# Kernel tuning notes

Hardware: AMD Instinct MI355X
Metric: run time of the kernel (lower is better)

The kernel has to match this reference:

```python
import jax, jax.numpy as jnp
import numpy as np
import functools

N, D, R, E, L, C, MAXDEG = 40000, 128, 3, 640000, 2, 40, 512
BN_EPS = 1e-5


def setup_inputs():
    ks = iter(jax.random.split(jax.random.key(0), 40))
    nrm = lambda s, sc=0.05: jax.random.normal(next(ks), s, dtype=jnp.float32) * sc
    x = jax.random.normal(next(ks), (N, D), dtype=jnp.float32)
    edge_indices = jax.random.randint(next(ks), (R, 2, E), 0, N, dtype=jnp.int32)
    out_emb = nrm((L, MAXDEG, D)).at[:, 0].set(0.0)  # padding_idx=0 -> zero row
    in_emb = nrm((L, MAXDEG, D)).at[:, 0].set(0.0)
    return dict(
        x=x, edge_indices=edge_indices,
        W_src=nrm((L, D, D)), b_src=nrm((L, D)),
        W_dst=nrm((L, D, D)), b_dst=nrm((L, D)),
        W_outf=nrm((L, D)), b_outf=nrm((L,)),
        W_inf=nrm((L, D)), b_inf=nrm((L,)),
        W_fc=nrm((L, D, D)), b_fc=nrm((L, D)),
        bn_gamma=jnp.ones((L, D), jnp.float32), bn_beta=jnp.zeros((L, D), jnp.float32),
        out_deg_emb=out_emb, in_deg_emb=in_emb,
        out_mask=jnp.ones((R, N), jnp.float32), out_mask_bias=jnp.zeros((R, N), jnp.float32),
        in_mask=jnp.ones((R, N), jnp.float32), in_mask_bias=jnp.zeros((R, N), jnp.float32),
        alpha=jnp.float32(0.5), tau=jnp.float32(0.0),
        W_lin=nrm((D, C)), b_lin=nrm((C,)),
    )


def _forward(x, W_src, b_src, W_dst, b_dst, W_outf, b_outf, W_inf, b_inf,
             W_fc, b_fc, bn_gamma, bn_beta, out_deg_emb, in_deg_emb,
             out_mask, out_mask_bias, in_mask, in_mask_bias, alpha, tau,
             W_lin, b_lin, edge_indices):
    seg = lambda d, i: jax.ops.segment_sum(d, i, num_segments=N)
    # source builds I with arange(0, N-1): identity with last diagonal entry missing
    i_mask = (jnp.arange(N) < N - 1).astype(jnp.float32)[:, None]

    rel = []
    for r in range(R):
        row, col = edge_indices[r, 0], edge_indices[r, 1]
        ones = jnp.ones(E, jnp.float32)
        out_deg, in_deg = seg(ones, row), seg(ones, col)
        ods = jnp.where(out_deg > 0, 1.0 / jnp.sqrt(jnp.maximum(out_deg, 1.0)), 0.0)
        ids_ = jnp.where(in_deg > 0, 1.0 / jnp.sqrt(jnp.maximum(in_deg, 1.0)), 0.0)
        # 'dir' norm: D_out^{-1/2} A D_in^{-1/2}; the transposed adj shares the same edge weights
        w = ods[row] * ids_[col]
        rel.append((row, col, w,
                    jnp.clip(out_deg, 0, MAXDEG - 1).astype(jnp.int32),
                    jnp.clip(in_deg, 0, MAXDEG - 1).astype(jnp.int32)))

    def spmm(r_, y):  # adj_norm @ y : gather cols, scatter-add to rows
        row, col, w = rel[r_][0], rel[r_][1], rel[r_][2]
        return seg(w[:, None] * y[col], row)

    def spmm_t(r_, y):  # adj_norm^T @ y
        row, col, w = rel[r_][0], rel[r_][1], rel[r_][2]
        return seg(w[:, None] * y[row], col)

    def dirichlet(mm, y):
        x1 = y / (jnp.sum(jnp.abs(y), axis=1, keepdims=True) + 1e-12)  # row_l1_normalize
        x1sq = x1 * x1
        return (i_mask * x1sq + mm(x1sq)) - 2.0 * ((i_mask * x1 + mm(x1)) * x1 - x1sq)

    eff_tau = jnp.exp(tau) + 0.1

    def conv(l, h):
        out = jnp.zeros((N, D), h.dtype)
        cis, cos_ = [], []
        for r in range(R):
            mm = functools.partial(spmm, r)
            mmt = functools.partial(spmm_t, r)
            out_nei, in_nei = mm(h), mmt(h)
            e_out, e_in = dirichlet(mm, h), dirichlet(mmt, h)
            c_out = (-e_out + out_deg_emb[l][rel[r][3]]) @ W_outf[l] + b_outf[l]  # [N]
            c_in = (-e_in + in_deg_emb[l][rel[r][4]]) @ W_inf[l] + b_inf[l]
            cm = jax.nn.softmax(jnp.stack([c_out, c_in], axis=1) / eff_tau, axis=1)  # tau_softmax
            c_out = cm[:, 0] * out_mask[r] + out_mask_bias[r]
            c_in = cm[:, 1] * in_mask[r] + in_mask_bias[r]
            out = out + c_out[:, None] * (out_nei @ W_src[l] + b_src[l]) \
                      + c_in[:, None] * (in_nei @ W_dst[l] + b_dst[l])
            cis.append(c_in)
            cos_.append(c_out)
        out = out / R
        # F.pad(x,(0,dim-x.shape[1])) is a no-op since input_dim == output_dim
        output = out + alpha * (h @ W_fc[l] + b_fc[l])
        mu, var = jnp.mean(output, axis=0), jnp.var(output, axis=0)  # BatchNorm1d (train mode)
        output = (output - mu) / jnp.sqrt(var + BN_EPS) * bn_gamma[l] + bn_beta[l]
        return output, jnp.mean(jnp.stack(cis), 0)[:, None], jnp.mean(jnp.stack(cos_), 0)[:, None]

    pos_h, neg_h = x, x
    pos_hs, neg_hs, gs, cins, couts = [], [], [], [], []
    for l in range(L):
        ph, ci, co = conv(l, pos_h)
        ph = jax.nn.relu(ph)  # jumping_knowledge truthy -> relu every layer; dropout p=0
        perm = jax.random.permutation(jax.random.key(100 + l), N)  # torch.randperm
        nh, _, _ = conv(l, neg_h[perm])
        nh = jax.nn.relu(nh)
        pos_h, neg_h = ph, nh
        pos_hs.append(ph)
        neg_hs.append(nh)
        gs.append(jnp.mean(ph, axis=0, keepdims=True))
        cins.append(ci)
        couts.append(co)
    c_ins = jnp.mean(jnp.stack(cins), 0)
    c_outs = jnp.mean(jnp.stack(couts), 0)
    jk = functools.reduce(jnp.maximum, pos_hs)  # JumpingKnowledge mode='max'
    logp = jax.nn.log_softmax(jk @ W_lin + b_lin, axis=1)
    return (logp, c_ins, c_outs, *pos_hs, *neg_hs, *gs)


def reference(x, edge_indices, W_src, b_src, W_dst, b_dst, W_outf, b_outf,
              W_inf, b_inf, W_fc, b_fc, bn_gamma, bn_beta, out_deg_emb,
              in_deg_emb, out_mask, out_mask_bias, in_mask, in_mask_bias,
              alpha, tau, W_lin, b_lin):
    return _forward(x, W_src, b_src, W_dst, b_dst, W_outf, b_outf, W_inf, b_inf,
                    W_fc, b_fc, bn_gamma, bn_beta, out_deg_emb, in_deg_emb,
                    out_mask, out_mask_bias, in_mask, in_mask_bias, alpha, tau,
                    W_lin, b_lin, edge_indices)
```

## Files before the change

kernel.cpp:

```cpp
#include <hip/hip_runtime.h>

constexpr int Nn = 40000;
constexpr int Dd = 128;
constexpr int Rr = 3;
constexpr int Ee = 640000;
constexpr int Ll = 2;
constexpr int Cc = 40;
constexpr int MAXD = 512;
constexpr float BN_EPS = 1e-5f;

constexpr int RB_ELEMS = 1024;
constexpr int RB_NB = (Nn + RB_ELEMS - 1) / RB_ELEMS;
constexpr int RB_BINS = 256;
constexpr int RB_H = RB_BINS * RB_NB;

constexpr int EB_ELEMS = 4096;
constexpr int EB_NB = (Ee + EB_ELEMS - 1) / EB_ELEMS;
constexpr int EB_H = 256 * EB_NB;

constexpr int HR_BINS = 13334;
constexpr int HR_PAD = 13344;
constexpr int HR_SB = 16;
constexpr int HR_CHUNK = (Ee + HR_SB - 1) / HR_SB;

__device__ __forceinline__ unsigned rotl32(unsigned x, int d) { return (x << d) | (x >> (32 - d)); }

__device__ void threefry2x32(unsigned k0, unsigned k1, unsigned c0, unsigned c1,
                             unsigned& o0, unsigned& o1) {
  unsigned ks2 = k0 ^ k1 ^ 0x1BD11BDAu;
  unsigned x0 = c0 + k0, x1 = c1 + k1;
#define TFR4(a,b,c,d2) \
  x0 += x1; x1 = rotl32(x1,a);  x1 ^= x0; \
  x0 += x1; x1 = rotl32(x1,b);  x1 ^= x0; \
  x0 += x1; x1 = rotl32(x1,c);  x1 ^= x0; \
  x0 += x1; x1 = rotl32(x1,d2); x1 ^= x0;
  TFR4(13,15,26,6);  x0 += k1;  x1 += ks2 + 1u;
  TFR4(17,29,16,24); x0 += ks2; x1 += k0 + 2u;
  TFR4(13,15,26,6);  x0 += k0;  x1 += k1 + 3u;
  TFR4(17,29,16,24); x0 += k1;  x1 += ks2 + 4u;
  TFR4(13,15,26,6);  x0 += ks2; x1 += k0 + 5u;
#undef TFR4
  o0 = x0; o1 = x1;
}

__global__ void k_genkeys2(unsigned* __restrict__ keys, unsigned seed0, unsigned seed1,
                           int rounds, int* __restrict__ vout, int doIota) {
  int i = blockIdx.x * blockDim.x + threadIdx.x;
  if (i >= 2 * Nn) return;
  int seg = i / Nn, li = i - seg * Nn;
  unsigned seed = seg ? seed1 : seed0;
  unsigned k0 = 0u, k1 = seed, sk0 = 0u, sk1 = 0u;
  for (int rd = 0; rd < rounds; rd++) {
    unsigned a0, a1, b0, b1;
    threefry2x32(k0, k1, 0u, 0u, a0, a1);
    threefry2x32(k0, k1, 0u, 1u, b0, b1);
    sk0 = b0; sk1 = b1;
    k0 = a0; k1 = a1;
  }
  unsigned o0, o1;
  threefry2x32(sk0, sk1, 0u, (unsigned)li, o0, o1);
  keys[i] = o0 ^ o1;
  if (doIota) vout[i] = li;
}

__global__ void k_rhist2(const unsigned* __restrict__ keys, int* __restrict__ hist, int shift) {
  __shared__ int lh[RB_BINS];
  int a = blockIdx.x / RB_NB, blk = blockIdx.x % RB_NB;
  const unsigned* src = keys + (size_t)a * Nn;
  int t = threadIdx.x;
  lh[t] = 0;
  __syncthreads();
  int base = blk * RB_ELEMS;
  for (int i = t; i < RB_ELEMS; i += 256) {
    int g = base + i;
    if (g < Nn) atomicAdd(&lh[(src[g] >> shift) & 255], 1);
  }
  __syncthreads();
  hist[(size_t)a * RB_H + t * RB_NB + blk] = lh[t];
}

__device__ void scan_body(const int* cnt, int* off, int n, int items) {
  int t = threadIdx.x;
  int lo = t * items, hi = min(lo + items, n);
  int s = 0;
  for (int i = lo; i < hi; i++) s += cnt[i];
  int lane = t & 63, wid = t >> 6;
  int sc = s;
#pragma unroll
  for (int o = 1; o < 64; o <<= 1) {
    int v = __shfl_up(sc, o);
    if (lane >= o) sc += v;
  }
  __shared__ int wsum[16], woff[16];
  if (lane == 63) wsum[wid] = sc;
  __syncthreads();
  if (t == 0) {
    int a = 0;
    for (int w = 0; w < 16; w++) { woff[w] = a; a += wsum[w]; }
    off[n] = a;
  }
  __syncthreads();
  int run = woff[wid] + sc - s;
  for (int i = lo; i < hi; i++) {
    int v = cnt[i];
    off[i] = run;
    run += v;
  }
}

__global__ __launch_bounds__(1024) void k_scanP(const int* __restrict__ hist, int* __restrict__ esc) {
  int a = blockIdx.x;
  scan_body(hist + (size_t)a * RB_H, esc + (size_t)a * (RB_H + 1), RB_H, (RB_H + 1023) / 1024);
}

__global__ __launch_bounds__(1024) void k_scan6(const int* __restrict__ odeg, const int* __restrict__ ideg,
                                                int* __restrict__ csr_off, int* __restrict__ csc_off) {
  int b = blockIdx.x;
  const int* cnt = (b < 3) ? (odeg + b * Nn) : (ideg + (b - 3) * Nn);
  int* off = (b < 3) ? (csr_off + b * (Nn + 1)) : (csc_off + (b - 3) * (Nn + 1));
  scan_body(cnt, off, Nn, (Nn + 1023) / 1024);
}

__global__ void k_rscatter2(const unsigned* __restrict__ keys, const int* __restrict__ vals,
                            const int* __restrict__ scanned, int shift,
                            unsigned* __restrict__ okeys, int* __restrict__ ovals) {
  __shared__ int running[RB_BINS];
  __shared__ int wcount[4][RB_BINS];
  __shared__ int dbase[RB_BINS];
  int a = blockIdx.x / RB_NB, blk = blockIdx.x % RB_NB;
  const unsigned* ksrc = keys + (size_t)a * Nn;
  const int* vsrc = vals + (size_t)a * Nn;
  unsigned* kdst = okeys + (size_t)a * Nn;
  int* vdst = ovals + (size_t)a * Nn;
  int t = threadIdx.x;
  int lane = t & 63, w = t >> 6;
  running[t] = 0;
  dbase[t] = scanned[(size_t)a * (RB_H + 1) + t * RB_NB + blk];
  int base = blk * RB_ELEMS;
  for (int rnd = 0; rnd < 4; rnd++) {
#pragma unroll
    for (int q = 0; q < 4; q++) wcount[q][t] = 0;
    __syncthreads();
    int g = base + rnd * 256 + t;
    bool valid = g < Nn;
    unsigned key = valid ? ksrc[g] : 0u;
    int d = (key >> shift) & 255;
    unsigned long long bb = __ballot(valid);
    unsigned long long mask = bb;
#pragma unroll
    for (int k = 0; k < 8; k++) {
      bool b = (d >> k) & 1;
      unsigned long long tt = __ballot(b && valid);
      mask &= b ? tt : ~tt;
    }
    mask &= bb;
    int riw = __popcll(mask & ((1ull << lane) - 1ull));
    int cnt_ = __popcll(mask);
    if (valid && riw == 0) wcount[w][d] = cnt_;
    __syncthreads();
    if (valid) {
      int prior = 0;
#pragma unroll
      for (int ww = 0; ww < 4; ww++) if (ww < w) prior += wcount[ww][d];
      int gp = dbase[d] + running[d] + prior + riw;
      kdst[gp] = key;
      vdst[gp] = vsrc[g];
    }
    __syncthreads();
    running[t] += wcount[0][t] + wcount[1][t] + wcount[2][t] + wcount[3][t];
    __syncthreads();
  }
}

__global__ void k_permrows(const float* __restrict__ src, const int* __restrict__ perm,
                           float* __restrict__ dst) {
  int row = blockIdx.x * 8 + (threadIdx.x >> 5);
  int lane = threadIdx.x & 31;
  if (row >= Nn) return;
  int p = perm[row];
  ((float4*)(dst + (size_t)row * Dd))[lane] = ((const float4*)(src + (size_t)p * Dd))[lane];
}

__global__ __launch_bounds__(256) void k_hist2(const int* __restrict__ ei, int* __restrict__ partials) {
  __shared__ int lh[HR_BINS];
  int bid = blockIdx.x;
  int sb = bid % HR_SB;
  int range = (bid / HR_SB) % 3;
  int j = bid / (3 * HR_SB);
  int rel = j >> 1, which = j & 1;
  const int* src = ei + (size_t)rel * 2 * Ee + (size_t)which * Ee;
  int lo = range * HR_BINS;
  for (int i = threadIdx.x; i < HR_BINS; i += 256) lh[i] = 0;
  __syncthreads();
  int e0 = sb * HR_CHUNK, e1 = min(e0 + HR_CHUNK, Ee);
  for (int e = e0 + threadIdx.x; e < e1; e += 256) {
    int v = src[e] - lo;
    if (v >= 0 && v < HR_BINS) atomicAdd(&lh[v], 1);
  }
  __syncthreads();
  int* dst = partials + (size_t)bid * HR_PAD;
  for (int i = threadIdx.x; i < HR_BINS; i += 256) dst[i] = lh[i];
}

__global__ void k_hreduce(const int* __restrict__ partials, int* __restrict__ odeg,
                          int* __restrict__ ideg) {
  int idx = blockIdx.x * 256 + threadIdx.x;
  if (idx >= 6 * Nn) return;
  int j = idx / Nn, bin = idx - j * Nn;
  int range = bin / HR_BINS, off = bin - range * HR_BINS;
  const int* p = partials + (size_t)((j * 3 + range) * HR_SB) * HR_PAD + off;
  int sum = 0;
#pragma unroll
  for (int b = 0; b < HR_SB; b++) sum += p[(size_t)b * HR_PAD];
  int rel = j >> 1;
  (j & 1 ? ideg : odeg)[rel * Nn + bin] = sum;
}

__global__ void k_degnorm(const int* __restrict__ odeg, const int* __restrict__ ideg,
                          float* __restrict__ ods, float* __restrict__ ids,
                          int* __restrict__ odix, int* __restrict__ idix) {
  int idx = blockIdx.x * blockDim.x + threadIdx.x;
  if (idx >= Rr * Nn) return;
  int od = odeg[idx], id_ = ideg[idx];
  ods[idx] = od > 0 ? 1.0f / sqrtf((float)od) : 0.0f;
  ids[idx] = id_ > 0 ? 1.0f / sqrtf((float)id_) : 0.0f;
  odix[idx] = od < MAXD - 1 ? od : MAXD - 1;
  idix[idx] = id_ < MAXD - 1 ? id_ : MAXD - 1;
}

__global__ void k_pack(const int* __restrict__ ei, unsigned* __restrict__ pcsr,
                       unsigned* __restrict__ pcsc) {
  int idx = blockIdx.x * 256 + threadIdx.x;
  if (idx >= 3 * Ee) return;
  int r = idx / Ee, e = idx - r * Ee;
  const int* base = ei + (size_t)r * 2 * Ee;
  unsigned rw = (unsigned)base[e], cl = (unsigned)base[Ee + e];
  pcsr[idx] = (rw << 16) | cl;
  pcsc[idx] = (cl << 16) | rw;
}

__global__ __launch_bounds__(256) void k_ehist(const unsigned* __restrict__ pin,
                                               int* __restrict__ hist, int shift) {
  __shared__ int lh[256];
  int a = blockIdx.x / EB_NB, blk = blockIdx.x % EB_NB;
  const unsigned* src = pin + (size_t)a * Ee;
  lh[threadIdx.x] = 0;
  __syncthreads();
  int base = blk * EB_ELEMS;
  for (int i = threadIdx.x; i < EB_ELEMS; i += 256) {
    int g = base + i;
    if (g < Ee) atomicAdd(&lh[(src[g] >> shift) & 255], 1);
  }
  __syncthreads();
  hist[(size_t)a * EB_H + threadIdx.x * EB_NB + blk] = lh[threadIdx.x];
}

__global__ __launch_bounds__(1024) void k_escan6(const int* __restrict__ hist, int* __restrict__ esc) {
  int a = blockIdx.x;
  scan_body(hist + (size_t)a * EB_H, esc + (size_t)a * (EB_H + 1), EB_H, (EB_H + 1023) / 1024);
}

__global__ __launch_bounds__(256) void k_escatter(const unsigned* __restrict__ pin,
                                                  const int* __restrict__ esc, int shift,
                                                  unsigned* __restrict__ pout) {
  __shared__ int running[256];
  __shared__ int wcount[4][256];
  __shared__ int dbase[256];
  int a = blockIdx.x / EB_NB, blk = blockIdx.x % EB_NB;
  const unsigned* src = pin + (size_t)a * Ee;
  unsigned* dst = pout + (size_t)a * Ee;
  int t = threadIdx.x;
  int lane = t & 63, w = t >> 6;
  running[t] = 0;
  dbase[t] = esc[(size_t)a * (EB_H + 1) + t * EB_NB + blk];
  int base = blk * EB_ELEMS;
  for (int rnd = 0; rnd < 16; rnd++) {
#pragma unroll
    for (int q = 0; q < 4; q++) wcount[q][t] = 0;
    __syncthreads();
    int g = base + rnd * 256 + t;
    bool valid = g < Ee;
    unsigned key = valid ? src[g] : 0u;
    int d = (key >> shift) & 255;
    unsigned long long bb = __ballot(valid);
    unsigned long long mask = bb;
#pragma unroll
    for (int k = 0; k < 8; k++) {
      bool b = (d >> k) & 1;
      unsigned long long tt = __ballot(b && valid);
      mask &= b ? tt : ~tt;
    }
    mask &= bb;
    int riw = __popcll(mask & ((1ull << lane) - 1ull));
    int cnt_ = __popcll(mask);
    if (valid && riw == 0) wcount[w][d] = cnt_;
    __syncthreads();
    if (valid) {
      int prior = 0;
#pragma unroll
      for (int ww = 0; ww < 4; ww++) if (ww < w) prior += wcount[ww][d];
      int gp = dbase[d] + running[d] + prior + riw;
      dst[gp] = key;
    }
    __syncthreads();
    running[t] += wcount[0][t] + wcount[1][t] + wcount[2][t] + wcount[3][t];
    __syncthreads();
  }
}

__global__ void k_rowscalar(const float* __restrict__ h, const float* __restrict__ Wfo,
                            const float* __restrict__ Wfi, float4* __restrict__ aux) {
  int wid = (blockIdx.x * blockDim.x + threadIdx.x) >> 6;
  int lane = threadIdx.x & 63;
  if (wid >= Nn) return;
  float2 a = ((const float2*)(h + (size_t)wid * Dd))[lane];
  float2 wo = ((const float2*)Wfo)[lane];
  float2 wi = ((const float2*)Wfi)[lane];
  float l1 = fabsf(a.x) + fabsf(a.y);
  float so = a.x * a.x * wo.x + a.y * a.y * wo.y;
  float si = a.x * a.x * wi.x + a.y * a.y * wi.y;
#pragma unroll
  for (int o = 32; o; o >>= 1) {
    l1 += __shfl_xor(l1, o);
    so += __shfl_xor(so, o);
    si += __shfl_xor(si, o);
  }
  if (lane == 0) {
    float ri = 1.0f / (l1 + 1e-12f);
    aux[wid] = make_float4(ri, ri * ri * so, ri * ri * si, 0.f);
  }
}

__global__ void k_lut(const float* __restrict__ eo, const float* __restrict__ ei_,
                      const float* __restrict__ Wfo, const float* __restrict__ Wfi,
                      float* __restrict__ luto, float* __restrict__ luti) {
  int wid = (blockIdx.x * blockDim.x + threadIdx.x) >> 6;
  int lane = threadIdx.x & 63;
  if (wid >= MAXD) return;
  float2 a = ((const float2*)(eo + (size_t)wid * Dd))[lane];
  float2 b = ((const float2*)(ei_ + (size_t)wid * Dd))[lane];
  float2 wo = ((const float2*)Wfo)[lane];
  float2 wi = ((const float2*)Wfi)[lane];
  float so = a.x * wo.x + a.y * wo.y;
  float si = b.x * wi.x + b.y * wi.y;
#pragma unroll
  for (int o = 32; o; o >>= 1) { so += __shfl_xor(so, o); si += __shfl_xor(si, o); }
  if (lane == 0) { luto[wid] = so; luti[wid] = si; }
}

__global__ __launch_bounds__(256) void k_csrdir3(
    const int* __restrict__ csr_off, const unsigned* __restrict__ pcsr,
    const int* __restrict__ csc_off, const unsigned* __restrict__ pcsc,
    const float* __restrict__ ods_r, const float* __restrict__ ids_r,
    const float4* __restrict__ aux, const float* __restrict__ h,
    const float* __restrict__ Wfo, const float* __restrict__ Wfi,
    const float* __restrict__ luto, const float* __restrict__ luti,
    const int* __restrict__ odix, const int* __restrict__ idix,
    const float* __restrict__ bo, const float* __restrict__ bi,
    const float* __restrict__ taup,
    const float* __restrict__ omask, const float* __restrict__ omaskb,
    const float* __restrict__ imask, const float* __restrict__ imaskb,
    float* __restrict__ Tout, float* __restrict__ Tin,
    float* __restrict__ sco, float* __restrict__ sci,
    float* __restrict__ co_acc, float* __restrict__ ci_acc,
    int first, int is_pos) {
  __shared__ float lq[4], lp[4], lc[4];
  int t = threadIdx.x;
  int wv = t >> 6, lane = t & 63;
  int dir = wv >> 1;
  int n = blockIdx.x * 2 + (wv & 1);
  const int* off = dir ? csc_off : csr_off;
  const unsigned* nbrp = dir ? pcsc : pcsr;
  const float* scn = dir ? ods_r : ids_r;
  float a_self = (dir ? ids_r : ods_r)[n];
  const float* Wf = dir ? Wfi : Wfo;
  int s0 = off[n], s1 = off[n + 1];
  int hl = lane & 31, half = lane >> 5;
  float4 wf4 = ((const float4*)Wf)[hl];
  float4 hn4 = ((const float4*)(h + (size_t)n * Dd))[hl];
  float rn = aux[n].x;
  float4 s = make_float4(0.f, 0.f, 0.f, 0.f);
  float4 pa = make_float4(0.f, 0.f, 0.f, 0.f);
  float qacc = 0.f;
  for (int base = s0; base < s1; base += 64) {
    int eidx = base + lane;
    bool valid = eidx < s1;
    int mi = valid ? (int)(nbrp[eidx] & 0xFFFFu) : 0;
    float4 av = valid ? aux[mi] : make_float4(0.f, 0.f, 0.f, 0.f);
    float scv = valid ? scn[mi] : 0.f;
    float qsel = dir ? av.z : av.y;
    int cnt = min(64, s1 - base);
#pragma unroll 4
    for (int j = half; j < cnt; j += 2) {
      int m = __shfl(mi, j);
      float sc = __shfl(scv, j);
      float rm = __shfl(av.x, j);
      float qv = __shfl(qsel, j);
      float w = a_self * sc;
      float wrm = w * rm;
      float4 hv = ((const float4*)(h + (size_t)m * Dd))[hl];
      s.x += w * hv.x; s.y += w * hv.y; s.z += w * hv.z; s.w += w * hv.w;
      pa.x += wrm * hv.x; pa.y += wrm * hv.y; pa.z += wrm * hv.z; pa.w += wrm * hv.w;
      qacc += w * qv;
    }
  }
  s.x += __shfl_xor(s.x, 32); s.y += __shfl_xor(s.y, 32);
  s.z += __shfl_xor(s.z, 32); s.w += __shfl_xor(s.w, 32);
  pa.x += __shfl_xor(pa.x, 32); pa.y += __shfl_xor(pa.y, 32);
  pa.z += __shfl_xor(pa.z, 32); pa.w += __shfl_xor(pa.w, 32);
  qacc += __shfl_xor(qacc, 32);
  float pd = rn * (hn4.x * wf4.x * pa.x + hn4.y * wf4.y * pa.y +
                   hn4.z * wf4.z * pa.z + hn4.w * wf4.w * pa.w);
#pragma unroll
  for (int o = 16; o; o >>= 1) pd += __shfl_xor(pd, o);
  if (lane == 0) { lq[wv] = qacc; lp[wv] = pd; }
  __syncthreads();
  if (t < 2) {
    int nn = blockIdx.x * 2 + t;
    float Qo_ = lq[t], Po_ = lp[t], Qi_ = lq[2 + t], Pi_ = lp[2 + t];
    float4 a2 = aux[nn];
    float im = (nn < Nn - 1) ? 1.0f : 0.0f;
    float so_ = luto[odix[nn]] + bo[0] - (Qo_ - 2.0f * Po_ + (2.0f - im) * a2.y);
    float si_ = luti[idix[nn]] + bi[0] - (Qi_ - 2.0f * Pi_ + (2.0f - im) * a2.z);
    float tt = expf(taup[0]) + 0.1f;
    float aa = so_ / tt, bb = si_ / tt;
    float mm = fmaxf(aa, bb);
    float ea = expf(aa - mm), eb = expf(bb - mm);
    float inv = 1.0f / (ea + eb);
    float co = ea * inv * omask[nn] + omaskb[nn];
    float ci = eb * inv * imask[nn] + imaskb[nn];
    lc[t] = co; lc[2 + t] = ci;
    if (first) { sco[nn] = co; sci[nn] = ci; }
    else       { sco[nn] += co; sci[nn] += ci; }
    if (is_pos) { co_acc[nn] += co; ci_acc[nn] += ci; }
  }
  __syncthreads();
  float c = lc[wv];
  if (lane < 32) {
    float* T = dir ? Tin : Tout;
    size_t o = (size_t)n * Dd;
    float4 v = make_float4(c * s.x, c * s.y, c * s.z, c * s.w);
    if (!first) {
      float4 old = ((const float4*)(T + o))[hl];
      v.x += old.x; v.y += old.y; v.z += old.z; v.w += old.w;
    }
    ((float4*)(T + o))[hl] = v;
  }
}

__global__ __launch_bounds__(256) void k_gemmconv(
    const float* __restrict__ Tout, const float* __restrict__ Tin, const float* __restrict__ h,
    const float* __restrict__ Wsrc, const float* __restrict__ Wdst, const float* __restrict__ Wfc,
    const float* __restrict__ bsrc, const float* __restrict__ bdst, const float* __restrict__ bfc,
    const float* __restrict__ sco, const float* __restrict__ sci,
    const float* __restrict__ alphap, float* __restrict__ pre, float* __restrict__ bnsum) {
  __shared__ float Asm[64][36];
  __shared__ float Bsm[32][132];
  __shared__ float lsum[128], lsum2[128];
  int t = threadIdx.x;
  int rg = t >> 5, cg = t & 31;
  int m0 = blockIdx.x * 64;
  int arow = t >> 2, aq = t & 3;
  float alpha = alphap[0];
  float acc[8][4];
#pragma unroll
  for (int r = 0; r < 8; r++)
#pragma unroll
    for (int c = 0; c < 4; c++) acc[r][c] = 0.f;
  for (int kt = 0; kt < 12; kt++) {
    int sec = kt >> 2, kc = (kt & 3) * 32;
    const float* Ap = sec == 0 ? Tout : (sec == 1 ? Tin : h);
    const float* Wp = sec == 0 ? Wsrc : (sec == 1 ? Wdst : Wfc);
    float sA = (sec == 2) ? alpha : (1.0f / (float)Rr);
    __syncthreads();
    {
      const float4* src = (const float4*)(Ap + (size_t)(m0 + arow) * Dd + kc + aq * 8);
      float4 v0 = src[0], v1 = src[1];
      float4* d0 = (float4*)&Asm[arow][aq * 8];
      d0[0] = make_float4(v0.x * sA, v0.y * sA, v0.z * sA, v0.w * sA);
      d0[1] = make_float4(v1.x * sA, v1.y * sA, v1.z * sA, v1.w * sA);
    }
#pragma unroll
    for (int j = 0; j < 4; j++) {
      int idx = t + j * 256;
      int k = idx >> 5, d4 = idx & 31;
      *(float4*)&Bsm[k][d4 * 4] = *(const float4*)(Wp + (size_t)(kc + k) * Dd + d4 * 4);
    }
    __syncthreads();
#pragma unroll
    for (int kk = 0; kk < 32; kk += 4) {
      float4 af[8], bf[4];
#pragma unroll
      for (int r = 0; r < 8; r++) af[r] = *(const float4*)&Asm[rg * 8 + r][kk];
#pragma unroll
      for (int j = 0; j < 4; j++) bf[j] = *(const float4*)&Bsm[kk + j][cg * 4];
#pragma unroll
      for (int r = 0; r < 8; r++) {
        const float* ap = (const float*)&af[r];
#pragma unroll
        for (int j = 0; j < 4; j++) {
          const float* bp = (const float*)&bf[j];
          acc[r][0] += ap[j] * bp[0];
          acc[r][1] += ap[j] * bp[1];
          acc[r][2] += ap[j] * bp[2];
          acc[r][3] += ap[j] * bp[3];
        }
      }
    }
  }
  float4 vb1 = *(const float4*)(bsrc + cg * 4);
  float4 vb2 = *(const float4*)(bdst + cg * 4);
  float4 vbf = *(const float4*)(bfc + cg * 4);
  float ps[4] = {0.f, 0.f, 0.f, 0.f}, ps2[4] = {0.f, 0.f, 0.f, 0.f};
#pragma unroll
  for (int r = 0; r < 8; r++) {
    int row = m0 + rg * 8 + r;
    size_t o = (size_t)row * Dd + cg * 4;
    float s1 = sco[row] * (1.0f / (float)Rr), s2 = sci[row] * (1.0f / (float)Rr);
    float4 v;
    v.x = acc[r][0] + s1 * vb1.x + s2 * vb2.x + alpha * vbf.x;
    v.y = acc[r][1] + s1 * vb1.y + s2 * vb2.y + alpha * vbf.y;
    v.z = acc[r][2] + s1 * vb1.z + s2 * vb2.z + alpha * vbf.z;
    v.w = acc[r][3] + s1 * vb1.w + s2 * vb2.w + alpha * vbf.w;
    *(float4*)(pre + o) = v;
    ps[0] += v.x; ps[1] += v.y; ps[2] += v.z; ps[3] += v.w;
    ps2[0] += v.x * v.x; ps2[1] += v.y * v.y; ps2[2] += v.z * v.z; ps2[3] += v.w * v.w;
  }
  if (t < 128) { lsum[t] = 0.f; lsum2[t] = 0.f; }
  __syncthreads();
#pragma unroll
  for (int j = 0; j < 4; j++) {
    atomicAdd(&lsum[cg * 4 + j], ps[j]);
    atomicAdd(&lsum2[cg * 4 + j], ps2[j]);
  }
  __syncthreads();
  if (t < 128) atomicAdd(&bnsum[t], lsum[t]);
  else if (t < 256) atomicAdd(&bnsum[t], lsum2[t - 128]);
}

__global__ void k_bnapply(const float* __restrict__ pre, const float* __restrict__ sums,
                          const float* __restrict__ gamma, const float* __restrict__ beta,
                          float* __restrict__ hout, float* __restrict__ gs, int do_gs) {
  __shared__ float ls[256];
  int c = threadIdx.x & 127, sub = threadIdx.x >> 7;
  float mu = sums[c] * (1.0f / (float)Nn);
  float var = sums[c + 128] * (1.0f / (float)Nn) - mu * mu;
  float sc = gamma[c] / sqrtf(var + BN_EPS);
  float bt = beta[c];
  float g = 0.f;
  for (int n = blockIdx.x * 2 + sub; n < Nn; n += gridDim.x * 2) {
    float v = (pre[(size_t)n * Dd + c] - mu) * sc + bt;
    v = fmaxf(v, 0.f);
    hout[(size_t)n * Dd + c] = v;
    g += v;
  }
  if (do_gs) {
    ls[threadIdx.x] = g;
    __syncthreads();
    if (sub == 0) atomicAdd(&gs[c], (ls[c] + ls[c + 128]) * (1.0f / (float)Nn));
  }
}

__global__ __launch_bounds__(64) void k_logp(const float* __restrict__ ph0, const float* __restrict__ ph1,
                      const float* __restrict__ Wlin, const float* __restrict__ blin,
                      const float* __restrict__ ci_acc, const float* __restrict__ co_acc,
                      float* __restrict__ cins, float* __restrict__ couts,
                      float* __restrict__ logp) {
  __shared__ float jk[Dd];
  __shared__ float lg[Cc];
  int n = blockIdx.x, t = threadIdx.x;
  if (t == 63) {
    cins[n] = ci_acc[n] * (1.0f / (float)(Ll * Rr));
    couts[n] = co_acc[n] * (1.0f / (float)(Ll * Rr));
  }
  for (int d = t; d < Dd; d += 64) jk[d] = fmaxf(ph0[(size_t)n * Dd + d], ph1[(size_t)n * Dd + d]);
  __syncthreads();
  if (t < Cc) {
    float acc = blin[t];
    for (int k = 0; k < Dd; k++) acc += jk[k] * Wlin[k * Cc + t];
    lg[t] = acc;
  }
  __syncthreads();
  float m = -1e30f;
  for (int c = 0; c < Cc; c++) m = fmaxf(m, lg[c]);
  float s = 0.f;
  for (int c = 0; c < Cc; c++) s += expf(lg[c] - m);
  float lse = m + logf(s);
  if (t < Cc) logp[(size_t)n * Cc + t] = lg[t] - lse;
}

extern "C" void kernel_launch(void* const* d_in, const int* in_sizes, int n_in,
                              void* d_out, int out_size, void* d_ws, size_t ws_size,
                              hipStream_t stream) {
  const float* x      = (const float*)d_in[0];
  const int*   ei     = (const int*)d_in[1];
  const float* W_src  = (const float*)d_in[2];
  const float* b_src  = (const float*)d_in[3];
  const float* W_dst  = (const float*)d_in[4];
  const float* b_dst  = (const float*)d_in[5];
  const float* W_outf = (const float*)d_in[6];
  const float* b_outf = (const float*)d_in[7];
  const float* W_inf  = (const float*)d_in[8];
  const float* b_inf  = (const float*)d_in[9];
  const float* W_fc   = (const float*)d_in[10];
  const float* b_fc   = (const float*)d_in[11];
  const float* gamma  = (const float*)d_in[12];
  const float* beta   = (const float*)d_in[13];
  const float* oemb   = (const float*)d_in[14];
  const float* iemb   = (const float*)d_in[15];
  const float* omask  = (const float*)d_in[16];
  const float* omaskb = (const float*)d_in[17];
  const float* imask  = (const float*)d_in[18];
  const float* imaskb = (const float*)d_in[19];
  const float* alphap = (const float*)d_in[20];
  const float* taup   = (const float*)d_in[21];
  const float* Wlin   = (const float*)d_in[22];
  const float* blin   = (const float*)d_in[23];

  float* out   = (float*)d_out;
  float* logp  = out;
  float* cins  = logp + (size_t)Nn * Cc;
  float* couts = cins + Nn;
  float* ph0   = couts + Nn;
  float* ph1   = ph0 + (size_t)Nn * Dd;
  float* nh0   = ph1 + (size_t)Nn * Dd;
  float* nh1   = nh0 + (size_t)Nn * Dd;
  float* gs0   = nh1 + (size_t)Nn * Dd;
  float* gs1   = gs0 + Dd;

  char* p = (char*)d_ws;
  auto alloc = [&](size_t bytes) -> void* {
    void* q = (void*)p;
    p += (bytes + 255) & ~(size_t)255;
    return q;
  };
  float* pre   = (float*)alloc((size_t)Nn * Dd * 4);
  float* Tout  = (float*)alloc((size_t)Nn * Dd * 4);
  float* Tin   = (float*)alloc((size_t)Nn * Dd * 4);
  float* hperm = (float*)alloc((size_t)Nn * Dd * 4);
  unsigned* pbuf = (unsigned*)alloc((size_t)6 * Ee * 4);
  size_t qwords = (size_t)6 * Ee;
  size_t pwords = (size_t)(6 * 3 * HR_SB) * HR_PAD;
  unsigned* qbuf = (unsigned*)alloc((qwords > pwords ? qwords : pwords) * 4);
  int* partials = (int*)qbuf;
  int* csr_off = (int*)alloc((size_t)Rr * (Nn + 1) * 4);
  int* csc_off = (int*)alloc((size_t)Rr * (Nn + 1) * 4);
  int* odeg    = (int*)alloc((size_t)Rr * Nn * 4);
  int* ideg    = (int*)alloc((size_t)Rr * Nn * 4);
  float* ods   = (float*)alloc((size_t)Rr * Nn * 4);
  float* ids   = (float*)alloc((size_t)Rr * Nn * 4);
  int* odix    = (int*)alloc((size_t)Rr * Nn * 4);
  int* idix    = (int*)alloc((size_t)Rr * Nn * 4);
  float4* aux  = (float4*)alloc((size_t)Nn * 16);
  float* sco   = (float*)alloc((size_t)Nn * 4 * 2);
  float* sci   = sco + Nn;
  float* coacc = (float*)alloc((size_t)Nn * 4 * 2);
  float* ciacc = coacc + Nn;
  float* luto  = (float*)alloc(MAXD * 4);
  float* luti  = (float*)alloc(MAXD * 4);
  float* bnsum = (float*)alloc(256 * 4);
  unsigned* kbuf0 = (unsigned*)alloc((size_t)2 * Nn * 4);
  unsigned* kbuf1 = (unsigned*)alloc((size_t)2 * Nn * 4);
  int* vbuf0 = (int*)alloc((size_t)2 * Nn * 4);
  int* vbuf1 = (int*)alloc((size_t)2 * Nn * 4);
  int* rhist = (int*)alloc((size_t)2 * (RB_H + 1) * 4);
  int* rscan = (int*)alloc((size_t)2 * (RB_H + 1) * 4);
  int* ehist = (int*)alloc((size_t)6 * EB_H * 4);
  int* escan = (int*)alloc((size_t)6 * (EB_H + 1) * 4);

  k_hist2<<<6 * 3 * HR_SB, 256, 0, stream>>>(ei, partials);
  k_hreduce<<<(6 * Nn + 255) / 256, 256, 0, stream>>>(partials, odeg, ideg);
  k_degnorm<<<(Rr * Nn + 255) / 256, 256, 0, stream>>>(odeg, ideg, ods, ids, odix, idix);
  k_scan6<<<6, 1024, 0, stream>>>(odeg, ideg, csr_off, csc_off);
  k_pack<<<(3 * Ee + 255) / 256, 256, 0, stream>>>(ei, pbuf, pbuf + (size_t)3 * Ee);
  k_ehist<<<6 * EB_NB, 256, 0, stream>>>(pbuf, ehist, 16);
  k_escan6<<<6, 1024, 0, stream>>>(ehist, escan);
  k_escatter<<<6 * EB_NB, 256, 0, stream>>>(pbuf, escan, 16, qbuf);
  k_ehist<<<6 * EB_NB, 256, 0, stream>>>(qbuf, ehist, 24);
  k_escan6<<<6, 1024, 0, stream>>>(ehist, escan);
  k_escatter<<<6 * EB_NB, 256, 0, stream>>>(qbuf, escan, 24, pbuf);
  hipMemsetAsync(coacc, 0, (size_t)Nn * 4 * 2, stream);

  auto radix4b = [&]() {
    for (int pass = 0; pass < 4; pass++) {
      const unsigned* ik = (pass & 1) ? kbuf1 : kbuf0;
      const int*      iv = (pass & 1) ? vbuf1 : vbuf0;
      unsigned*       ok = (pass & 1) ? kbuf0 : kbuf1;
      int*            ov = (pass & 1) ? vbuf0 : vbuf1;
      int shift = pass * 8;
      k_rhist2<<<2 * RB_NB, 256, 0, stream>>>(ik, rhist, shift);
      k_scanP<<<2, 1024, 0, stream>>>(rhist, rscan);
      k_rscatter2<<<2 * RB_NB, 256, 0, stream>>>(ik, iv, rscan, shift, ok, ov);
    }
  };
  k_genkeys2<<<(2 * Nn + 255) / 256, 256, 0, stream>>>(kbuf0, 100u, 101u, 1, vbuf0, 1);
  radix4b();
  k_genkeys2<<<(2 * Nn + 255) / 256, 256, 0, stream>>>(kbuf0, 100u, 101u, 2, vbuf0, 0);
  radix4b();

  auto conv = [&](int l, const float* hin, float* hout, float* gs, int is_pos) {
    const float* Wfo = W_outf + l * Dd;
    const float* Wfi = W_inf + l * Dd;
    k_rowscalar<<<Nn / 4, 256, 0, stream>>>(hin, Wfo, Wfi, aux);
    for (int r = 0; r < Rr; r++) {
      k_csrdir3<<<Nn / 2, 256, 0, stream>>>(csr_off + r * (Nn + 1), pbuf + (size_t)r * Ee,
                                            csc_off + r * (Nn + 1), pbuf + (size_t)(3 + r) * Ee,
                                            ods + r * Nn, ids + r * Nn, aux, hin, Wfo, Wfi,
                                            luto, luti, odix + r * Nn, idix + r * Nn,
                                            b_outf + l, b_inf + l, taup,
                                            omask + (size_t)r * Nn, omaskb + (size_t)r * Nn,
                                            imask + (size_t)r * Nn, imaskb + (size_t)r * Nn,
                                            Tout, Tin, sco, sci, coacc, ciacc,
                                            r == 0 ? 1 : 0, is_pos);
    }
    hipMemsetAsync(bnsum, 0, 256 * 4, stream);
    k_gemmconv<<<Nn / 64, 256, 0, stream>>>(Tout, Tin, hin,
                                            W_src + (size_t)l * Dd * Dd, W_dst + (size_t)l * Dd * Dd,
                                            W_fc + (size_t)l * Dd * Dd,
                                            b_src + l * Dd, b_dst + l * Dd, b_fc + l * Dd,
                                            sco, sci, alphap, pre, bnsum);
    if (is_pos) hipMemsetAsync(gs, 0, Dd * 4, stream);
    k_bnapply<<<256, 256, 0, stream>>>(pre, bnsum, gamma + l * Dd, beta + l * Dd, hout, gs, is_pos);
  };

  k_lut<<<MAXD / 4, 256, 0, stream>>>(oemb, iemb, W_outf, W_inf, luto, luti);
  conv(0, x, ph0, gs0, 1);
  k_permrows<<<Nn / 8, 256, 0, stream>>>(x, vbuf0, hperm);
  conv(0, hperm, nh0, nullptr, 0);

  k_lut<<<MAXD / 4, 256, 0, stream>>>(oemb + (size_t)MAXD * Dd, iemb + (size_t)MAXD * Dd,
                                      W_outf + Dd, W_inf + Dd, luto, luti);
  conv(1, ph0, ph1, gs1, 1);
  k_permrows<<<Nn / 8, 256, 0, stream>>>(nh0, vbuf0 + Nn, hperm);
  conv(1, hperm, nh1, nullptr, 0);

  k_logp<<<Nn, 64, 0, stream>>>(ph0, ph1, Wlin, blin, ciacc, coacc, cins, couts, logp);
}
```

Baseline: 2.232 ms.

## Pack per-relation neighbor scalars, fold memsets into rowscalar, prefetch GEMM tiles

k_rowscalar now also writes per-relation, per-direction packed float4 arrays holding the degree scale, row L1 reciprocal and selected q value. The edge-aggregation kernel then does one float4 gather per neighbor instead of a float4 gather plus a separate scalar gather. The bnsum and gs memsets move into rowscalar, and both layers' LUTs are computed in a single launch up front. The GEMM kernel register-prefetches the next A/B tile while computing the current one. The cost is extra writes of 6*N float4 per conv and higher register pressure in the GEMM.

```diff
diff --git a/kernel.cpp b/kernel.cpp
--- a/kernel.cpp
+++ b/kernel.cpp
@@ -309,7 +309,14 @@
 }
 
 __global__ void k_rowscalar(const float* __restrict__ h, const float* __restrict__ Wfo,
-                            const float* __restrict__ Wfi, float4* __restrict__ aux) {
+                            const float* __restrict__ Wfi, float4* __restrict__ aux,
+                            const float* __restrict__ ods, const float* __restrict__ ids,
+                            float4* __restrict__ auxrd,
+                            float* __restrict__ bnsum, float* __restrict__ gs) {
+  if (blockIdx.x == 0) {
+    bnsum[threadIdx.x] = 0.f;
+    if (gs != nullptr && threadIdx.x < Dd) gs[threadIdx.x] = 0.f;
+  }
   int wid = (blockIdx.x * blockDim.x + threadIdx.x) >> 6;
   int lane = threadIdx.x & 63;
   if (wid >= Nn) return;
@@ -327,20 +334,27 @@
   }
   if (lane == 0) {
     float ri = 1.0f / (l1 + 1e-12f);
-    aux[wid] = make_float4(ri, ri * ri * so, ri * ri * si, 0.f);
-  }
-}
-
-__global__ void k_lut(const float* __restrict__ eo, const float* __restrict__ ei_,
-                      const float* __restrict__ Wfo, const float* __restrict__ Wfi,
-                      float* __restrict__ luto, float* __restrict__ luti) {
+    float qo = ri * ri * so, qi = ri * ri * si;
+    aux[wid] = make_float4(ri, qo, qi, 0.f);
+#pragma unroll
+    for (int r = 0; r < Rr; r++) {
+      auxrd[(size_t)(2 * r) * Nn + wid] = make_float4(ids[r * Nn + wid], ri, qo, 0.f);
+      auxrd[(size_t)(2 * r + 1) * Nn + wid] = make_float4(ods[r * Nn + wid], ri, qi, 0.f);
+    }
+  }
+}
+
+__global__ void k_lut2(const float* __restrict__ eo, const float* __restrict__ ei_,
+                       const float* __restrict__ W_outf, const float* __restrict__ W_inf,
+                       float* __restrict__ luto, float* __restrict__ luti) {
   int wid = (blockIdx.x * blockDim.x + threadIdx.x) >> 6;
   int lane = threadIdx.x & 63;
-  if (wid >= MAXD) return;
-  float2 a = ((const float2*)(eo + (size_t)wid * Dd))[lane];
-  float2 b = ((const float2*)(ei_ + (size_t)wid * Dd))[lane];
-  float2 wo = ((const float2*)Wfo)[lane];
-  float2 wi = ((const float2*)Wfi)[lane];
+  if (wid >= 2 * MAXD) return;
+  int l = wid >> 9, k = wid & (MAXD - 1);
+  float2 a = ((const float2*)(eo + ((size_t)l * MAXD + k) * Dd))[lane];
+  float2 b = ((const float2*)(ei_ + ((size_t)l * MAXD + k) * Dd))[lane];
+  float2 wo = ((const float2*)(W_outf + l * Dd))[lane];
+  float2 wi = ((const float2*)(W_inf + l * Dd))[lane];
   float so = a.x * wo.x + a.y * wo.y;
   float si = b.x * wi.x + b.y * wi.y;
 #pragma unroll
@@ -352,6 +366,7 @@
     const int* __restrict__ csr_off, const unsigned* __restrict__ pcsr,
     const int* __restrict__ csc_off, const unsigned* __restrict__ pcsc,
     const float* __restrict__ ods_r, const float* __restrict__ ids_r,
+    const float4* __restrict__ auxo, const float4* __restrict__ auxi,
     const float4* __restrict__ aux, const float* __restrict__ h,
     const float* __restrict__ Wfo, const float* __restrict__ Wfi,
     const float* __restrict__ luto, const float* __restrict__ luti,
@@ -371,7 +386,7 @@
   int n = blockIdx.x * 2 + (wv & 1);
   const int* off = dir ? csc_off : csr_off;
   const unsigned* nbrp = dir ? pcsc : pcsr;
-  const float* scn = dir ? ods_r : ids_r;
+  const float4* auxd = dir ? auxi : auxo;
   float a_self = (dir ? ids_r : ods_r)[n];
   const float* Wf = dir ? Wfi : Wfo;
   int s0 = off[n], s1 = off[n + 1];
@@ -386,16 +401,14 @@
     int eidx = base + lane;
     bool valid = eidx < s1;
     int mi = valid ? (int)(nbrp[eidx] & 0xFFFFu) : 0;
-    float4 av = valid ? aux[mi] : make_float4(0.f, 0.f, 0.f, 0.f);
-    float scv = valid ? scn[mi] : 0.f;
-    float qsel = dir ? av.z : av.y;
+    float4 av = valid ? auxd[mi] : make_float4(0.f, 0.f, 0.f, 0.f);
     int cnt = min(64, s1 - base);
 #pragma unroll 4
     for (int j = half; j < cnt; j += 2) {
       int m = __shfl(mi, j);
-      float sc = __shfl(scv, j);
-      float rm = __shfl(av.x, j);
-      float qv = __shfl(qsel, j);
+      float sc = __shfl(av.x, j);
+      float rm = __shfl(av.y, j);
+      float qv = __shfl(av.z, j);
       float w = a_self * sc;
       float wrm = w * rm;
       float4 hv = ((const float4*)(h + (size_t)m * Dd))[hl];
@@ -467,24 +480,46 @@
   for (int r = 0; r < 8; r++)
 #pragma unroll
     for (int c = 0; c < 4; c++) acc[r][c] = 0.f;
-  for (int kt = 0; kt < 12; kt++) {
+  int bk = (t + 0) >> 5;
+  auto aptr = [&](int kt) -> const float4* {
     int sec = kt >> 2, kc = (kt & 3) * 32;
     const float* Ap = sec == 0 ? Tout : (sec == 1 ? Tin : h);
+    return (const float4*)(Ap + (size_t)(m0 + arow) * Dd + kc + aq * 8);
+  };
+  auto bptr = [&](int kt, int j) -> const float4* {
+    int sec = kt >> 2, kc = (kt & 3) * 32;
     const float* Wp = sec == 0 ? Wsrc : (sec == 1 ? Wdst : Wfc);
-    float sA = (sec == 2) ? alpha : (1.0f / (float)Rr);
+    int idx = t + j * 256;
+    int k = idx >> 5, d4 = idx & 31;
+    return (const float4*)(Wp + (size_t)(kc + k) * Dd + d4 * 4);
+  };
+  float4 ra0, ra1, rb[4];
+  {
+    const float4* ap = aptr(0);
+    ra0 = ap[0]; ra1 = ap[1];
+#pragma unroll
+    for (int j = 0; j < 4; j++) rb[j] = *bptr(0, j);
+  }
+  for (int kt = 0; kt < 12; kt++) {
+    float sA = (kt >= 8) ? alpha : (1.0f / (float)Rr);
     __syncthreads();
     {
-      const float4* src = (const float4*)(Ap + (size_t)(m0 + arow) * Dd + kc + aq * 8);
-      float4 v0 = src[0], v1 = src[1];
       float4* d0 = (float4*)&Asm[arow][aq * 8];
-      d0[0] = make_float4(v0.x * sA, v0.y * sA, v0.z * sA, v0.w * sA);
-      d0[1] = make_float4(v1.x * sA, v1.y * sA, v1.z * sA, v1.w * sA);
-    }
-#pragma unroll
-    for (int j = 0; j < 4; j++) {
-      int idx = t + j * 256;
-      int k = idx >> 5, d4 = idx & 31;
-      *(float4*)&Bsm[k][d4 * 4] = *(const float4*)(Wp + (size_t)(kc + k) * Dd + d4 * 4);
+      d0[0] = make_float4(ra0.x * sA, ra0.y * sA, ra0.z * sA, ra0.w * sA);
+      d0[1] = make_float4(ra1.x * sA, ra1.y * sA, ra1.z * sA, ra1.w * sA);
+#pragma unroll
+      for (int j = 0; j < 4; j++) {
+        int idx = t + j * 256;
+        int k = idx >> 5, d4 = idx & 31;
+        *(float4*)&Bsm[k][d4 * 4] = rb[j];
+      }
+    }
+    float4 na0, na1, nb[4];
+    if (kt < 11) {
+      const float4* ap = aptr(kt + 1);
+      na0 = ap[0]; na1 = ap[1];
+#pragma unroll
+      for (int j = 0; j < 4; j++) nb[j] = *bptr(kt + 1, j);
     }
     __syncthreads();
 #pragma unroll
@@ -507,7 +542,13 @@
         }
       }
     }
-  }
+    if (kt < 11) {
+      ra0 = na0; ra1 = na1;
+#pragma unroll
+      for (int j = 0; j < 4; j++) rb[j] = nb[j];
+    }
+  }
+  (void)bk;
   float4 vb1 = *(const float4*)(bsrc + cg * 4);
   float4 vb2 = *(const float4*)(bdst + cg * 4);
   float4 vbf = *(const float4*)(bfc + cg * 4);
@@ -652,12 +693,13 @@
   int* odix    = (int*)alloc((size_t)Rr * Nn * 4);
   int* idix    = (int*)alloc((size_t)Rr * Nn * 4);
   float4* aux  = (float4*)alloc((size_t)Nn * 16);
+  float4* auxrd = (float4*)alloc((size_t)6 * Nn * 16);
   float* sco   = (float*)alloc((size_t)Nn * 4 * 2);
   float* sci   = sco + Nn;
   float* coacc = (float*)alloc((size_t)Nn * 4 * 2);
   float* ciacc = coacc + Nn;
-  float* luto  = (float*)alloc(MAXD * 4);
-  float* luti  = (float*)alloc(MAXD * 4);
+  float* luto  = (float*)alloc((size_t)2 * MAXD * 4);
+  float* luti  = (float*)alloc((size_t)2 * MAXD * 4);
   float* bnsum = (float*)alloc(256 * 4);
   unsigned* kbuf0 = (unsigned*)alloc((size_t)2 * Nn * 4);
   unsigned* kbuf1 = (unsigned*)alloc((size_t)2 * Nn * 4);
@@ -680,6 +722,7 @@
   k_escan6<<<6, 1024, 0, stream>>>(ehist, escan);
   k_escatter<<<6 * EB_NB, 256, 0, stream>>>(qbuf, escan, 24, pbuf);
   hipMemsetAsync(coacc, 0, (size_t)Nn * 4 * 2, stream);
+  k_lut2<<<2 * MAXD / 4, 256, 0, stream>>>(oemb, iemb, W_outf, W_inf, luto, luti);
 
   auto radix4b = [&]() {
     for (int pass = 0; pass < 4; pass++) {
@@ -701,35 +744,35 @@
   auto conv = [&](int l, const float* hin, float* hout, float* gs, int is_pos) {
     const float* Wfo = W_outf + l * Dd;
     const float* Wfi = W_inf + l * Dd;
-    k_rowscalar<<<Nn / 4, 256, 0, stream>>>(hin, Wfo, Wfi, aux);
+    k_rowscalar<<<Nn / 4, 256, 0, stream>>>(hin, Wfo, Wfi, aux, ods, ids, auxrd, bnsum,
+                                            is_pos ? gs : nullptr);
     for (int r = 0; r < Rr; r++) {
       k_csrdir3<<<Nn / 2, 256, 0, stream>>>(csr_off + r * (Nn + 1), pbuf + (size_t)r * Ee,
                                             csc_off + r * (Nn + 1), pbuf + (size_t)(3 + r) * Ee,
-                                            ods + r * Nn, ids + r * Nn, aux, hin, Wfo, Wfi,
-                                            luto, luti, odix + r * Nn, idix + r * Nn,
+                                            ods + r * Nn, ids + r * Nn,
+                                            auxrd + (size_t)(2 * r) * Nn,
+                                            auxrd + (size_t)(2 * r + 1) * Nn,
+                                            aux, hin, Wfo, Wfi,
+                                            luto + l * MAXD, luti + l * MAXD,
+                                            odix + r * Nn, idix + r * Nn,
                                             b_outf + l, b_inf + l, taup,
                                             omask + (size_t)r * Nn, omaskb + (size_t)r * Nn,
                                             imask + (size_t)r * Nn, imaskb + (size_t)r * Nn,
                                             Tout, Tin, sco, sci, coacc, ciacc,
                                             r == 0 ? 1 : 0, is_pos);
     }
-    hipMemsetAsync(bnsum, 0, 256 * 4, stream);
     k_gemmconv<<<Nn / 64, 256, 0, stream>>>(Tout, Tin, hin,
                                             W_src + (size_t)l * Dd * Dd, W_dst + (size_t)l * Dd * Dd,
                                             W_fc + (size_t)l * Dd * Dd,
                                             b_src + l * Dd, b_dst + l * Dd, b_fc + l * Dd,
                                             sco, sci, alphap, pre, bnsum);
-    if (is_pos) hipMemsetAsync(gs, 0, Dd * 4, stream);
     k_bnapply<<<256, 256, 0, stream>>>(pre, bnsum, gamma + l * Dd, beta + l * Dd, hout, gs, is_pos);
   };
 
-  k_lut<<<MAXD / 4, 256, 0, stream>>>(oemb, iemb, W_outf, W_inf, luto, luti);
   conv(0, x, ph0, gs0, 1);
   k_permrows<<<Nn / 8, 256, 0, stream>>>(x, vbuf0, hperm);
   conv(0, hperm, nh0, nullptr, 0);
 
-  k_lut<<<MAXD / 4, 256, 0, stream>>>(oemb + (size_t)MAXD * Dd, iemb + (size_t)MAXD * Dd,
-                                      W_outf + Dd, W_inf + Dd, luto, luti);
   conv(1, ph0, ph1, gs1, 1);
   k_permrows<<<Nn / 8, 256, 0, stream>>>(nh0, vbuf0 + Nn, hperm);
   conv(1, hperm, nh1, nullptr, 0);
```

Result: slower. 2.732 ms (+22.4%).
